# Performance work log

Hardware: AMD Instinct MI355X
Metric: run time of the kernel (lower is better)

The kernel has to match this reference:

```python
import jax, jax.numpy as jnp
import numpy as np

N_NODES = 100_000
N_EDGES = 1_600_000
DIM_IN = 256
ADD_TO_EDGE_SCORE = 0.5  # PyG EdgePooling default


def setup_inputs() -> dict:
    key = jax.random.key(0)
    k1, k2, k3 = jax.random.split(key, 3)
    x = jax.random.normal(k1, (N_NODES, DIM_IN), dtype=jnp.float32)
    edge_index = jax.random.randint(k2, (2, N_EDGES), 0, N_NODES, dtype=jnp.int32)
    batch = jnp.zeros((N_NODES,), dtype=jnp.int32)  # single graph
    W = jax.random.normal(k3, (2 * DIM_IN, 1), dtype=jnp.float32) / np.sqrt(2.0 * DIM_IN)
    b = jnp.zeros((1,), dtype=jnp.float32)
    return {"x": x, "edge_index": edge_index, "batch": batch, "W": W, "b": b}


def _segment_softmax(scores, seg, num_segments):
    m = jax.ops.segment_max(scores, seg, num_segments=num_segments)
    ex = jnp.exp(scores - m[seg])
    s = jax.ops.segment_sum(ex, seg, num_segments=num_segments)
    return ex / s[seg]


def _greedy_matching(rank, src, dst, num_nodes):
    """Maximal matching equivalent to sequential greedy over edges sorted by
    ascending rank (rank = position in descending-score argsort, a strict total
    order). Implemented as parallel locally-dominant matching rounds."""
    big = jnp.iinfo(jnp.int32).max

    def cond(state):
        alive, matched, chosen = state
        return jnp.any(alive)

    def body(state):
        alive, matched, chosen = state
        r = jnp.where(alive, rank, big)
        node_min = jnp.full((num_nodes,), big, dtype=jnp.int32)
        node_min = node_min.at[src].min(r)
        node_min = node_min.at[dst].min(r)
        # an alive edge is picked if it dominates all alive edges at both endpoints
        pick = alive & (rank == node_min[src]) & (rank == node_min[dst])
        matched = matched.at[jnp.where(pick, src, num_nodes)].set(True, mode='drop')
        matched = matched.at[jnp.where(pick, dst, num_nodes)].set(True, mode='drop')
        chosen = chosen | pick
        alive = alive & ~matched[src] & ~matched[dst]
        return alive, matched, chosen

    alive0 = jnp.ones_like(rank, dtype=bool)
    matched0 = jnp.zeros((num_nodes,), dtype=bool)
    chosen0 = jnp.zeros_like(alive0)
    _, matched, chosen = jax.lax.while_loop(cond, body, (alive0, matched0, chosen0))
    return chosen, matched


def reference(x, edge_index, batch, W, b):
    num_nodes, feat = x.shape
    num_edges = edge_index.shape[1]
    src, dst = edge_index[0], edge_index[1]

    # Linear([x_src || x_dst]) split to avoid materializing [E, 2F]
    s_src = x @ W[:feat, 0]   # [N]
    s_dst = x @ W[feat:, 0]   # [N]
    raw = s_src[src] + s_dst[dst] + b[0]            # [E]
    # dropout is identity in eval mode
    e = _segment_softmax(raw, dst, num_nodes) + ADD_TO_EDGE_SCORE  # [E]

    # rank: position of each edge in descending-score order
    order = jnp.argsort(-e)
    rank = jnp.zeros((num_edges,), dtype=jnp.int32).at[order].set(
        jnp.arange(num_edges, dtype=jnp.int32))

    chosen, matched = _greedy_matching(rank, src, dst, num_nodes)

    # cluster id of each chosen edge = its position among chosen edges in score order
    chosen_sorted = chosen[order]
    cid_sorted = jnp.cumsum(chosen_sorted.astype(jnp.int32)) - 1
    cid = jnp.zeros((num_edges,), dtype=jnp.int32).at[order].set(cid_sorted)
    num_matched = jnp.sum(chosen.astype(jnp.int32))

    # node -> cluster assignment; unmatched nodes get trailing singleton clusters
    cluster = jnp.zeros((num_nodes,), dtype=jnp.int32)
    cluster = cluster.at[jnp.where(chosen, src, num_nodes)].set(cid, mode='drop')
    cluster = cluster.at[jnp.where(chosen, dst, num_nodes)].set(cid, mode='drop')
    unm = num_matched + jnp.cumsum((~matched).astype(jnp.int32)) - 1
    cluster = jnp.where(matched, cluster, unm)
    num_clusters = num_matched + jnp.sum((~matched).astype(jnp.int32))

    # per-cluster score: chosen-edge scores for merged pairs, 1.0 for singletons
    new_edge_score = jnp.ones((num_nodes,), dtype=x.dtype)
    new_edge_score = new_edge_score.at[jnp.where(chosen, cid, num_nodes)].set(e, mode='drop')

    # scatter-merge node features (rows >= num_clusters are zero padding)
    new_x = jax.ops.segment_sum(x, cluster, num_segments=num_nodes)
    new_x = new_x * new_edge_score[:, None]

    new_edge_index = cluster[edge_index]  # remapped edges (coalesce/dedup omitted)
    new_batch = jnp.zeros((num_nodes,), dtype=batch.dtype).at[cluster].set(batch)

    return new_x, new_edge_index, new_batch, num_clusters
```

## Files before the change

### kernel.cpp

```cpp
#include <hip/hip_runtime.h>

typedef unsigned int u32;
typedef unsigned long long u64;
typedef unsigned char u8;

static constexpr int SORTN = 65536;
static constexpr int STILE = 2048;
static constexpr int NR    = 20;
static constexpr int NHEAVY= 3;
static constexpr int NXCD  = 8;

__device__ __forceinline__ u32 xccid() {
  u32 x;
  asm volatile("s_getreg_b32 %0, hwreg(HW_REG_XCC_ID)" : "=s"(x));
  return x & (NXCD - 1);
}

__device__ __forceinline__ void wmin64(u64* p, u64 v) {
  __hip_atomic_fetch_min(p, v, __ATOMIC_RELAXED, __HIP_MEMORY_SCOPE_WORKGROUP);
}
__device__ __forceinline__ void waddf64(double* p, double v) {
  __hip_atomic_fetch_add(p, v, __ATOMIC_RELAXED, __HIP_MEMORY_SCOPE_WORKGROUP);
}

typedef __attribute__((ext_vector_type(4))) float evf4;
template <typename T>
__device__ __forceinline__ T ntl(const T* p) { return __builtin_nontemporal_load(p); }
template <typename T>
__device__ __forceinline__ void nts(T v, T* p) { __builtin_nontemporal_store(v, p); }
__device__ __forceinline__ float4 ntl4(const float4* p) {
  evf4 v = __builtin_nontemporal_load((const evf4*)p);
  return make_float4(v.x, v.y, v.z, v.w);
}
__device__ __forceinline__ void nts4(float4 v, float4* p) {
  evf4 t; t.x = v.x; t.y = v.y; t.z = v.z; t.w = v.w;
  __builtin_nontemporal_store(t, (evf4*)p);
}

__device__ __forceinline__ u32 ordf(float f) {
  u32 u = __float_as_uint(f);
  return (u & 0x80000000u) ? ~u : (u | 0x80000000u);
}
__device__ __forceinline__ float inv_ordf(u32 m) {
  return __uint_as_float((m & 0x80000000u) ? (m ^ 0x80000000u) : ~m);
}

__global__ __launch_bounds__(256)
void k_init(double* ssum, double* ss8, u8* matched,
            u64* node_min, u64* nm8, float* scoreC, ulonglong2* sortbuf,
            u32* fcnt, u32* scalars, int N, int E) {
  int i = blockIdx.x * blockDim.x + threadIdx.x;
  if (i < N) { ssum[i] = 0.0; matched[i] = 0; scoreC[i] = 1.0f; }
  if (i < 2 * N) node_min[i] = ~0ull;
  if (i < NXCD * N) { nm8[i] = ~0ull; ss8[i] = 0.0; }
  if (i < SORTN) sortbuf[i] = make_ulonglong2(~0ull, ~0ull);
  if (i < 256)   fcnt[i] = 0u;
  if (i < 16)    scalars[i] = 0u;
  if (i == 0)    fcnt[0] = (u32)E;
}

__global__ __launch_bounds__(256)
void k_dots(const float4* __restrict__ x4, const float4* __restrict__ W4,
            float* __restrict__ s_src, float* __restrict__ s_dst, int N) {
  int gt = blockIdx.x * blockDim.x + threadIdx.x;
  int w = gt >> 6, lane = gt & 63;
  if (w >= N) return;
  float4 xa = ntl4(&x4[(size_t)w * 64 + lane]);
  float4 wa = W4[lane];
  float4 wb = W4[64 + lane];
  float pa = xa.x*wa.x + xa.y*wa.y + xa.z*wa.z + xa.w*wa.w;
  float pb = xa.x*wb.x + xa.y*wb.y + xa.z*wb.z + xa.w*wb.w;
  #pragma unroll
  for (int m = 32; m >= 1; m >>= 1) {
    pa += __shfl_xor(pa, m);
    pb += __shfl_xor(pb, m);
  }
  if (lane == 0) { s_src[w] = pa; s_dst[w] = pb; }
}

__global__ __launch_bounds__(256)
void k_esum(const int* __restrict__ src, const int* __restrict__ dst,
            const float* __restrict__ s_src, const float* __restrict__ s_dst,
            const float* __restrict__ bvec, double* ss8,
            float* __restrict__ exv, u64* __restrict__ frontS, int N, int E) {
  int e = blockIdx.x * blockDim.x + threadIdx.x;
  if (e >= E) return;
  double* sW = ss8 + (size_t)xccid() * N;
  int s = ntl(&src[e]), d = ntl(&dst[e]);
  float r = s_src[s] + s_dst[d] + bvec[0];
  float ex = expf(r);
  nts(ex, &exv[e]);
  nts(((u64)(u32)s << 32) | (u32)d, &frontS[e]);
  waddf64(&sW[d], (double)ex);
}

__global__ __launch_bounds__(256)
void k_ssmerge(const double* __restrict__ ss8, double* __restrict__ ssum, int N) {
  int v = blockIdx.x * 256 + threadIdx.x;
  if (v >= N) return;
  double s = 0.0;
  #pragma unroll
  for (int x = 0; x < NXCD; x++) s += ss8[(size_t)x * N + v];
  ssum[v] = s;
}

__global__ __launch_bounds__(256)
void k_scorekey(const u64* __restrict__ frontS, const float* __restrict__ exv,
                const double* __restrict__ ssum,
                u64* __restrict__ frontK, u64* nm8, int N, int E) {
  int e = blockIdx.x * blockDim.x + threadIdx.x;
  if (e >= E) return;
  u64* nmW = nm8 + (size_t)xccid() * N;
  u64 sd = ntl(&frontS[e]);
  int s = (int)(sd >> 32), d = (int)(u32)sd;
  float es = ntl(&exv[e]) / (float)ssum[d] + 0.5f;
  u64 key = ((u64)(~ordf(es)) << 32) | (u32)e;
  nts(key, &frontK[e]);
  wmin64(&nmW[s], key);
  if (d != s) wmin64(&nmW[d], key);
}

__global__ __launch_bounds__(256)
void k_merge(u64* nm8, u64* __restrict__ nmOut, int N) {
  int v = blockIdx.x * 256 + threadIdx.x;
  if (v >= N) return;
  u64 m = ~0ull;
  #pragma unroll
  for (int x = 0; x < NXCD; x++) {
    size_t idx = (size_t)x * N + v;
    u64 t = nm8[idx];
    if (t != ~0ull) { nm8[idx] = ~0ull; m = (t < m) ? t : m; }
  }
  nmOut[v] = m;
}

template<int R>
__global__ __launch_bounds__(256)
void k_mmin_h(const u64* __restrict__ fK, const u64* __restrict__ fS,
              const u32* __restrict__ cntp, const u8* __restrict__ matched,
              u64* nm8, int N) {
  u32 cnt = *cntp;
  u64* nmW = nm8 + (size_t)xccid() * N;
  u32 nth = gridDim.x * 256;
  for (u32 i = blockIdx.x * 256 + threadIdx.x; i < cnt; i += nth) {
    u64 sd = ntl(&fS[i]);
    int s = (int)(sd >> 32), d = (int)(u32)sd;
    if (matched[s] | matched[d]) continue;
    u64 k = ntl(&fK[i]);
    wmin64(&nmW[s], k);
    if (d != s) wmin64(&nmW[d], k);
  }
}

template<int R>
__global__ __launch_bounds__(256)
void k_mmin_l(const u64* __restrict__ fK, const u64* __restrict__ fS,
              const u32* __restrict__ cntp, const u8* __restrict__ matched,
              u64* nm) {
  u32 cnt = *cntp;
  u32 nth = gridDim.x * 256;
  for (u32 i = blockIdx.x * 256 + threadIdx.x; i < cnt; i += nth) {
    u64 sd = ntl(&fS[i]);
    int s = (int)(sd >> 32), d = (int)(u32)sd;
    if (matched[s] | matched[d]) continue;
    u64 k = ntl(&fK[i]);
    atomicMin(&nm[s], k);
    if (d != s) atomicMin(&nm[d], k);
  }
}

template<int R>
__global__ __launch_bounds__(256)
void k_mpick(const u64* __restrict__ fKin, const u64* __restrict__ fSin,
             const u32* __restrict__ cntp, const u64* __restrict__ nm,
             u64* nmNext, u8* matched, u64* fKout, u64* fSout, u32* cntOut,
             ulonglong2* sortbuf, u32* scalars) {
  __shared__ u32 wb[4];
  __shared__ u32 bbase;
  u32 cnt = *cntp;
  int tx = threadIdx.x, lane = tx & 63, wid = tx >> 6;
  for (u32 base = blockIdx.x * 256; base < cnt; base += gridDim.x * 256) {
    u32 gid = base + tx;
    u64 k = 0, sd = 0;
    int s = 0, d = 0;
    bool pk = false, surv = false;
    if (gid < cnt) {
      k = ntl(&fKin[gid]); sd = ntl(&fSin[gid]);
      s = (int)(sd >> 32); d = (int)(u32)sd;
      if (!(matched[s] | matched[d])) {
        pk = (nm[s] == k) && (nm[d] == k);
        surv = !pk;
      }
    }
    u64 pm = __ballot(pk);
    if (pm) {
      u32 pre = (u32)__popcll(pm & ((1ull << lane) - 1ull));
      int ldr = __ffsll((long long)pm) - 1;
      u32 pb = 0;
      if (lane == ldr) pb = atomicAdd(&scalars[0], (u32)__popcll(pm));
      pb = __shfl(pb, ldr);
      if (pk) { matched[s] = 1; matched[d] = 1; sortbuf[pb + pre] = make_ulonglong2(k, sd); }
    }
    u64 sm = __ballot(surv);
    if (lane == 0) wb[wid] = (u32)__popcll(sm);
    __syncthreads();
    if (tx == 0) {
      u32 tt = wb[0] + wb[1] + wb[2] + wb[3];
      bbase = tt ? atomicAdd(cntOut, tt) : 0u;
    }
    __syncthreads();
    if (surv) {
      u32 woff = 0;
      for (int w = 0; w < wid; w++) woff += wb[w];
      u32 pre = (u32)__popcll(sm & ((1ull << lane) - 1ull));
      u32 o = bbase + woff + pre;
      nts(k, &fKout[o]);
      nts(sd, &fSout[o]);
      nmNext[s] = ~0ull;
      if (d != s) nmNext[d] = ~0ull;
    }
    __syncthreads();
  }
}

__global__ __launch_bounds__(1024)
void k_mfinish(u64* fKA, u64* fSA, u64* fKB, u64* fSB, u8* matched,
               u64* nmA, u64* nmB, ulonglong2* sortbuf,
               const u32* __restrict__ cntp, u32* scalars) {
  __shared__ u32 sh_cnt;
  u32 cnt = *cntp;
  int tx = threadIdx.x;
  u64 *fKin = fKA, *fSin = fSA, *fKout = fKB, *fSout = fSB;
  u64 *nmCur = nmA, *nmNxt = nmB;
  while (cnt > 0) {
    if (tx == 0) sh_cnt = 0;
    __syncthreads();
    for (u32 i = tx; i < cnt; i += 1024) {
      u64 sd = fSin[i];
      int s = (int)(sd >> 32), d = (int)(u32)sd;
      if (matched[s] | matched[d]) continue;
      u64 k = fKin[i];
      wmin64(&nmCur[s], k);
      if (d != s) wmin64(&nmCur[d], k);
    }
    __syncthreads();
    for (u32 i = tx; i < cnt; i += 1024) {
      u64 sd = fSin[i];
      int s = (int)(sd >> 32), d = (int)(u32)sd;
      if (matched[s] | matched[d]) continue;
      u64 k = fKin[i];
      u64 a = __hip_atomic_fetch_add(&nmCur[s], 0ull, __ATOMIC_RELAXED,
                                     __HIP_MEMORY_SCOPE_WORKGROUP);
      u64 b = (d == s) ? a
            : __hip_atomic_fetch_add(&nmCur[d], 0ull, __ATOMIC_RELAXED,
                                     __HIP_MEMORY_SCOPE_WORKGROUP);
      if (a == k && b == k) {
        matched[s] = 1; matched[d] = 1;
        u32 o = atomicAdd(&scalars[0], 1u);
        sortbuf[o] = make_ulonglong2(k, sd);
      } else {
        u32 o = atomicAdd(&sh_cnt, 1u);
        fKout[o] = k; fSout[o] = sd;
        nmNxt[s] = ~0ull;
        if (d != s) nmNxt[d] = ~0ull;
      }
    }
    __syncthreads();
    cnt = sh_cnt;
    u64* t;
    t = fKin; fKin = fKout; fKout = t;
    t = fSin; fSin = fSout; fSout = t;
    t = nmCur; nmCur = nmNxt; nmNxt = t;
    __syncthreads();
  }
}

__global__ __launch_bounds__(1024)
void k_sort1(ulonglong2* buf) {
  __shared__ ulonglong2 t[STILE];
  const int base = blockIdx.x * STILE;
  for (int i = threadIdx.x; i < STILE; i += 1024) t[i] = buf[base + i];
  __syncthreads();
  for (int k = 2; k <= STILE; k <<= 1) {
    for (int j = k >> 1; j > 0; j >>= 1) {
      for (int i = threadIdx.x; i < STILE; i += 1024) {
        int p = i ^ j;
        if (p > i) {
          bool dir = (((base + i) & k) == 0);
          ulonglong2 a = t[i], c = t[p];
          if ((a.x > c.x) == dir) { t[i] = c; t[p] = a; }
        }
      }
      __syncthreads();
    }
  }
  for (int i = threadIdx.x; i < STILE; i += 1024) buf[base + i] = t[i];
}

__global__ __launch_bounds__(256)
void k_gpass(ulonglong2* buf, int j, int k) {
  int i = blockIdx.x * 256 + threadIdx.x;
  int p = i ^ j;
  if (p > i && p < SORTN) {
    bool dir = ((i & k) == 0);
    ulonglong2 a = buf[i], c = buf[p];
    if ((a.x > c.x) == dir) { buf[i] = c; buf[p] = a; }
  }
}

__global__ __launch_bounds__(1024)
void k_sortl(ulonglong2* buf, int k) {
  __shared__ ulonglong2 t[STILE];
  const int base = blockIdx.x * STILE;
  const bool dir = ((base & k) == 0);
  for (int i = threadIdx.x; i < STILE; i += 1024) t[i] = buf[base + i];
  __syncthreads();
  for (int j = STILE >> 1; j > 0; j >>= 1) {
    for (int i = threadIdx.x; i < STILE; i += 1024) {
      int p = i ^ j;
      if (p > i) {
        ulonglong2 a = t[i], c = t[p];
        if ((a.x > c.x) == dir) { t[i] = c; t[p] = a; }
      }
    }
    __syncthreads();
  }
  for (int i = threadIdx.x; i < STILE; i += 1024) buf[base + i] = t[i];
}

__global__ __launch_bounds__(256)
void k_assign(const ulonglong2* __restrict__ buf,
              int* cluster, int* memA, int* memB, float* scoreC,
              const u32* __restrict__ scalars) {
  int i = blockIdx.x * blockDim.x + threadIdx.x;
  if (i >= (int)scalars[0]) return;
  ulonglong2 t = buf[i];
  int s = (int)(t.y >> 32), d = (int)(u32)t.y;
  cluster[s] = i; cluster[d] = i;
  scoreC[i] = inv_ordf(~(u32)(t.x >> 32));
  memA[i] = s;
  memB[i] = (s == d) ? -1 : d;
}

__global__ __launch_bounds__(256)
void k_scan1(const u8* __restrict__ matched, u32* partials, int N) {
  __shared__ u32 sh[256];
  int b = blockIdx.x, tx = threadIdx.x;
  int v0 = b * 1024 + tx * 4;
  u32 c = 0;
  #pragma unroll
  for (int q = 0; q < 4; q++) { int v = v0 + q; if (v < N && !matched[v]) c++; }
  sh[tx] = c; __syncthreads();
  for (int s = 128; s > 0; s >>= 1) { if (tx < s) sh[tx] += sh[tx + s]; __syncthreads(); }
  if (tx == 0) partials[b] = sh[0];
}

__global__ void k_scan2(const u32* partials, u32* partials2, u32* scalars, int NB) {
  if (blockIdx.x == 0 && threadIdx.x == 0) {
    u32 run = 0;
    for (int i = 0; i < NB; i++) { partials2[i] = run; run += partials[i]; }
    scalars[1] = run;
    scalars[2] = scalars[0] + run;
  }
}

__global__ __launch_bounds__(256)
void k_scan3(const u8* __restrict__ matched, const u32* __restrict__ partials2,
             const u32* __restrict__ scalars, int* cluster, int* memA, int* memB, int N) {
  __shared__ u32 sh[256];
  int b = blockIdx.x, tx = threadIdx.x;
  int v0 = b * 1024 + tx * 4;
  u32 f[4]; u32 c = 0;
  #pragma unroll
  for (int q = 0; q < 4; q++) { int v = v0 + q; f[q] = (v < N && !matched[v]); c += f[q]; }
  sh[tx] = c; __syncthreads();
  for (int s = 1; s < 256; s <<= 1) {
    u32 x = sh[tx];
    u32 y = (tx >= s) ? sh[tx - s] : 0;
    __syncthreads();
    sh[tx] = x + y;
    __syncthreads();
  }
  u32 base = scalars[0] + partials2[b] + (sh[tx] - c);
  #pragma unroll
  for (int q = 0; q < 4; q++) {
    if (f[q]) {
      int v = v0 + q;
      int cc = (int)base++;
      cluster[v] = cc; memA[cc] = v; memB[cc] = -1;
    }
  }
}

__global__ __launch_bounds__(256)
void k_newx(const float4* __restrict__ x4, const int* __restrict__ memA,
            const int* __restrict__ memB, const float* __restrict__ scoreC,
            const u32* __restrict__ scalars, float4* __restrict__ out4, int N) {
  int gt = blockIdx.x * blockDim.x + threadIdx.x;
  int w = gt >> 6, lane = gt & 63;
  if (w >= N) return;
  int nc = (int)scalars[2];
  float4 o;
  if (w < nc) {
    int a = memA[w], b = memB[w];
    float s = scoreC[w];
    float4 va = ntl4(&x4[(size_t)a * 64 + lane]);
    float ox = va.x, oy = va.y, oz = va.z, ow = va.w;
    if (b >= 0) {
      float4 vb = ntl4(&x4[(size_t)b * 64 + lane]);
      ox += vb.x; oy += vb.y; oz += vb.z; ow += vb.w;
    }
    o = make_float4(ox * s, oy * s, oz * s, ow * s);
  } else {
    o = make_float4(0.f, 0.f, 0.f, 0.f);
  }
  nts4(o, &out4[(size_t)w * 64 + lane]);
}

__global__ __launch_bounds__(256)
void k_remap(const int* __restrict__ ei, const int* __restrict__ cluster,
             float* __restrict__ outE, float* __restrict__ outB,
             const u32* __restrict__ scalars, int twoE, int N) {
  int i = blockIdx.x * blockDim.x + threadIdx.x;
  if (i < twoE) nts((float)cluster[ntl(&ei[i])], &outE[i]);
  int j = i - twoE;
  if (j >= 0 && j < N) outB[j] = 0.0f;
  if (j == N) outB[N] = (float)scalars[2];
}

template<int R>
static void launch_rounds(u64* fKA, u64* fSA, u64* fKB, u64* fSB, u64* nm8,
                          u64* node_min, u8* matched, ulonglong2* sortbuf,
                          u32* fcnt, u32* scalars, int N, int NB_E,
                          hipStream_t stream) {
  if constexpr (R < NR) {
    u64* fKin  = (R & 1) ? fKB : fKA;
    u64* fSin  = (R & 1) ? fSB : fSA;
    u64* fKout = (R & 1) ? fKA : fKB;
    u64* fSout = (R & 1) ? fSA : fSB;
    u64* nm  = node_min + (size_t)(R & 1) * N;
    u64* nmN = node_min + (size_t)((R & 1) ^ 1) * N;
    int nbr = (R < 30) ? (NB_E >> R) : 0; if (nbr < 64) nbr = 64;
    if constexpr (R == 0) {
    } else if constexpr (R < NHEAVY) {
      k_mmin_h<R><<<nbr, 256, 0, stream>>>(fKin, fSin, fcnt + R, matched, nm8, N);
      k_merge<<<(N + 255) / 256, 256, 0, stream>>>(nm8, nm, N);
    } else {
      k_mmin_l<R><<<nbr, 256, 0, stream>>>(fKin, fSin, fcnt + R, matched, nm);
    }
    k_mpick<R><<<nbr, 256, 0, stream>>>(fKin, fSin, fcnt + R, nm, nmN, matched,
                                        fKout, fSout, fcnt + R + 1, sortbuf, scalars);
    launch_rounds<R + 1>(fKA, fSA, fKB, fSB, nm8, node_min, matched, sortbuf,
                         fcnt, scalars, N, NB_E, stream);
  }
}

extern "C" void kernel_launch(void* const* d_in, const int* in_sizes, int n_in,
                              void* d_out, int out_size, void* d_ws, size_t ws_size,
                              hipStream_t stream) {
  const float* x    = (const float*)d_in[0];
  const int*   ei   = (const int*)d_in[1];
  const float* W    = (const float*)d_in[3];
  const float* bvec = (const float*)d_in[4];
  int N = in_sizes[2];
  int E = in_sizes[1] / 2;

  char* p = (char*)d_ws;
  auto alloc = [&](size_t bytes) { char* r = p; p += (bytes + 255) & ~(size_t)255; return r; };
  float*      s_src    = (float*)alloc((size_t)N * 4);
  float*      s_dst    = (float*)alloc((size_t)N * 4);
  double*     ssum     = (double*)alloc((size_t)N * 8);
  double*     ss8      = (double*)alloc((size_t)NXCD * N * 8);
  float*      exv      = (float*)alloc((size_t)E * 4);
  u64*        fKA      = (u64*)alloc((size_t)E * 8);
  u64*        fSA      = (u64*)alloc((size_t)E * 8);
  u64*        fKB      = (u64*)alloc((size_t)E * 8);
  u64*        fSB      = (u64*)alloc((size_t)E * 8);
  u8*         matched  = (u8*)alloc((size_t)N);
  u64*        node_min = (u64*)alloc((size_t)2 * N * 8);
  u64*        nm8      = (u64*)alloc((size_t)NXCD * N * 8);
  ulonglong2* sortbuf  = (ulonglong2*)alloc((size_t)SORTN * 16);
  int*        cluster  = (int*)alloc((size_t)N * 4);
  int*        memA     = (int*)alloc((size_t)N * 4);
  int*        memB     = (int*)alloc((size_t)N * 4);
  float*      scoreC   = (float*)alloc((size_t)N * 4);
  u32*        fcnt     = (u32*)alloc(1024);
  u32*        partials = (u32*)alloc(4096);
  u32*        partials2= (u32*)alloc(4096);
  u32*        scalars  = (u32*)alloc(256);
  (void)ws_size; (void)out_size; (void)n_in;

  const int* srcp = ei;
  const int* dstp = ei + E;
  float* out  = (float*)d_out;
  float* outX = out;
  float* outE = out + (size_t)N * 256;
  float* outB = outE + (size_t)2 * E;

  int NB_E = (E + 255) / 256;
  int cover = NXCD * N; if (cover < SORTN) cover = SORTN;
  k_init<<<(cover + 255) / 256, 256, 0, stream>>>(ssum, ss8, matched,
                                                  node_min, nm8, scoreC, sortbuf,
                                                  fcnt, scalars, N, E);
  k_dots<<<((size_t)N * 64 + 255) / 256, 256, 0, stream>>>(
      (const float4*)x, (const float4*)W, s_src, s_dst, N);
  k_esum<<<NB_E, 256, 0, stream>>>(srcp, dstp, s_src, s_dst, bvec, ss8,
                                   exv, fSA, N, E);
  k_ssmerge<<<(N + 255) / 256, 256, 0, stream>>>(ss8, ssum, N);
  k_scorekey<<<NB_E, 256, 0, stream>>>(fSA, exv, ssum, fKA, nm8, N, E);
  k_merge<<<(N + 255) / 256, 256, 0, stream>>>(nm8, node_min, N);

  launch_rounds<0>(fKA, fSA, fKB, fSB, nm8, node_min, matched, sortbuf,
                   fcnt, scalars, N, NB_E, stream);
  k_mfinish<<<1, 1024, 0, stream>>>(fKA, fSA, fKB, fSB, matched,
                                    node_min, node_min + N,
                                    sortbuf, fcnt + NR, scalars);

  k_sort1<<<SORTN / STILE, 1024, 0, stream>>>(sortbuf);
  for (int k = STILE << 1; k <= SORTN; k <<= 1) {
    for (int j = k >> 1; j >= STILE; j >>= 1)
      k_gpass<<<SORTN / 256, 256, 0, stream>>>(sortbuf, j, k);
    k_sortl<<<SORTN / STILE, 1024, 0, stream>>>(sortbuf, k);
  }

  k_assign<<<SORTN / 256, 256, 0, stream>>>(sortbuf, cluster, memA, memB, scoreC, scalars);
  int NB = (N + 1023) / 1024;
  k_scan1<<<NB, 256, 0, stream>>>(matched, partials, N);
  k_scan2<<<1, 64, 0, stream>>>(partials, partials2, scalars, NB);
  k_scan3<<<NB, 256, 0, stream>>>(matched, partials2, scalars, cluster, memA, memB, N);

  k_newx<<<((size_t)N * 64 + 255) / 256, 256, 0, stream>>>(
      (const float4*)x, memA, memB, scoreC, scalars, (float4*)outX, N);
  k_remap<<<(2 * E + N + 1 + 255) / 256, 256, 0, stream>>>(
      ei, cluster, outE, outB, scalars, 2 * E, N);
}
```

Baseline: 1.357 ms.

## Recompute edge keys on the fly and pack src/dst/id into one frontier word

Stops materializing the per-edge exp values and the separate key and src/dst frontier arrays. Edge scores are recomputed from the per-node dot products and softmax sums wherever a key is needed, and the frontier becomes one 64-bit word packing src (bits 38+), dst (17 bits) and edge id (21 bits). Round 0 reads edge_index directly, and the scan2 kernel is folded into scan3 so each block sums the partials itself. This removes several E-sized streams of writes and reads in exchange for repeated gathers, exp and divide per round. The packing assumes node ids fit in 17 bits and edge ids in 21 bits, which holds for the given sizes only.

```diff
diff --git a/kernel.cpp b/kernel.cpp
--- a/kernel.cpp
+++ b/kernel.cpp
@@ -9,6 +9,10 @@
 static constexpr int NR    = 20;
 static constexpr int NHEAVY= 3;
 static constexpr int NXCD  = 8;
+
+__device__ __forceinline__ u64 packsde(int s, int d, u32 e) {
+  return ((u64)(u32)s << 38) | ((u64)(u32)d << 21) | e;
+}
 
 __device__ __forceinline__ u32 xccid() {
   u32 x;
@@ -43,6 +47,13 @@
 }
 __device__ __forceinline__ float inv_ordf(u32 m) {
   return __uint_as_float((m & 0x80000000u) ? (m ^ 0x80000000u) : ~m);
+}
+
+__device__ __forceinline__ u64 edge_key(int s, int d, u32 e,
+    const float* __restrict__ s_src, const float* __restrict__ s_dst,
+    float b, const double* __restrict__ ssum) {
+  float es = expf(s_src[s] + s_dst[d] + b) / (float)ssum[d] + 0.5f;
+  return ((u64)(~ordf(es)) << 32) | e;
 }
 
 __global__ __launch_bounds__(256)
@@ -56,7 +67,6 @@
   if (i < SORTN) sortbuf[i] = make_ulonglong2(~0ull, ~0ull);
   if (i < 256)   fcnt[i] = 0u;
   if (i < 16)    scalars[i] = 0u;
-  if (i == 0)    fcnt[0] = (u32)E;
 }
 
 __global__ __launch_bounds__(256)
@@ -81,16 +91,12 @@
 __global__ __launch_bounds__(256)
 void k_esum(const int* __restrict__ src, const int* __restrict__ dst,
             const float* __restrict__ s_src, const float* __restrict__ s_dst,
-            const float* __restrict__ bvec, double* ss8,
-            float* __restrict__ exv, u64* __restrict__ frontS, int N, int E) {
+            const float* __restrict__ bvec, double* ss8, int N, int E) {
   int e = blockIdx.x * blockDim.x + threadIdx.x;
   if (e >= E) return;
   double* sW = ss8 + (size_t)xccid() * N;
   int s = ntl(&src[e]), d = ntl(&dst[e]);
-  float r = s_src[s] + s_dst[d] + bvec[0];
-  float ex = expf(r);
-  nts(ex, &exv[e]);
-  nts(((u64)(u32)s << 32) | (u32)d, &frontS[e]);
+  float ex = expf(s_src[s] + s_dst[d] + bvec[0]);
   waddf64(&sW[d], (double)ex);
 }
 
@@ -105,17 +111,15 @@
 }
 
 __global__ __launch_bounds__(256)
-void k_scorekey(const u64* __restrict__ frontS, const float* __restrict__ exv,
-                const double* __restrict__ ssum,
-                u64* __restrict__ frontK, u64* nm8, int N, int E) {
+void k_keymin(const int* __restrict__ src, const int* __restrict__ dst,
+              const float* __restrict__ s_src, const float* __restrict__ s_dst,
+              const float* __restrict__ bvec, const double* __restrict__ ssum,
+              u64* nm8, int N, int E) {
   int e = blockIdx.x * blockDim.x + threadIdx.x;
   if (e >= E) return;
   u64* nmW = nm8 + (size_t)xccid() * N;
-  u64 sd = ntl(&frontS[e]);
-  int s = (int)(sd >> 32), d = (int)(u32)sd;
-  float es = ntl(&exv[e]) / (float)ssum[d] + 0.5f;
-  u64 key = ((u64)(~ordf(es)) << 32) | (u32)e;
-  nts(key, &frontK[e]);
+  int s = ntl(&src[e]), d = ntl(&dst[e]);
+  u64 key = edge_key(s, d, (u32)e, s_src, s_dst, bvec[0], ssum);
   wmin64(&nmW[s], key);
   if (d != s) wmin64(&nmW[d], key);
 }
@@ -136,17 +140,20 @@
 
 template<int R>
 __global__ __launch_bounds__(256)
-void k_mmin_h(const u64* __restrict__ fK, const u64* __restrict__ fS,
-              const u32* __restrict__ cntp, const u8* __restrict__ matched,
+void k_mmin_h(const u64* __restrict__ fin, const u32* __restrict__ cntp,
+              const u8* __restrict__ matched,
+              const float* __restrict__ s_src, const float* __restrict__ s_dst,
+              const float* __restrict__ bvec, const double* __restrict__ ssum,
               u64* nm8, int N) {
   u32 cnt = *cntp;
   u64* nmW = nm8 + (size_t)xccid() * N;
   u32 nth = gridDim.x * 256;
+  float b = bvec[0];
   for (u32 i = blockIdx.x * 256 + threadIdx.x; i < cnt; i += nth) {
-    u64 sd = ntl(&fS[i]);
-    int s = (int)(sd >> 32), d = (int)(u32)sd;
+    u64 p = ntl(&fin[i]);
+    int s = (int)(p >> 38), d = (int)((p >> 21) & 0x1FFFF);
     if (matched[s] | matched[d]) continue;
-    u64 k = ntl(&fK[i]);
+    u64 k = edge_key(s, d, (u32)(p & 0x1FFFFF), s_src, s_dst, b, ssum);
     wmin64(&nmW[s], k);
     if (d != s) wmin64(&nmW[d], k);
   }
@@ -154,16 +161,19 @@
 
 template<int R>
 __global__ __launch_bounds__(256)
-void k_mmin_l(const u64* __restrict__ fK, const u64* __restrict__ fS,
-              const u32* __restrict__ cntp, const u8* __restrict__ matched,
+void k_mmin_l(const u64* __restrict__ fin, const u32* __restrict__ cntp,
+              const u8* __restrict__ matched,
+              const float* __restrict__ s_src, const float* __restrict__ s_dst,
+              const float* __restrict__ bvec, const double* __restrict__ ssum,
               u64* nm) {
   u32 cnt = *cntp;
   u32 nth = gridDim.x * 256;
+  float b = bvec[0];
   for (u32 i = blockIdx.x * 256 + threadIdx.x; i < cnt; i += nth) {
-    u64 sd = ntl(&fS[i]);
-    int s = (int)(sd >> 32), d = (int)(u32)sd;
+    u64 p = ntl(&fin[i]);
+    int s = (int)(p >> 38), d = (int)((p >> 21) & 0x1FFFF);
     if (matched[s] | matched[d]) continue;
-    u64 k = ntl(&fK[i]);
+    u64 k = edge_key(s, d, (u32)(p & 0x1FFFFF), s_src, s_dst, b, ssum);
     atomicMin(&nm[s], k);
     if (d != s) atomicMin(&nm[d], k);
   }
@@ -171,23 +181,32 @@
 
 template<int R>
 __global__ __launch_bounds__(256)
-void k_mpick(const u64* __restrict__ fKin, const u64* __restrict__ fSin,
-             const u32* __restrict__ cntp, const u64* __restrict__ nm,
-             u64* nmNext, u8* matched, u64* fKout, u64* fSout, u32* cntOut,
-             ulonglong2* sortbuf, u32* scalars) {
+void k_mpick(const int* __restrict__ src, const int* __restrict__ dst,
+             const u64* __restrict__ fin, const u32* __restrict__ cntp,
+             const float* __restrict__ s_src, const float* __restrict__ s_dst,
+             const float* __restrict__ bvec, const double* __restrict__ ssum,
+             const u64* __restrict__ nm, u64* nmNext, u8* matched,
+             u64* fout, u32* cntOut, ulonglong2* sortbuf, u32* scalars, int E) {
   __shared__ u32 wb[4];
   __shared__ u32 bbase;
-  u32 cnt = *cntp;
+  u32 cnt = (R == 0) ? (u32)E : *cntp;
+  float b = bvec[0];
   int tx = threadIdx.x, lane = tx & 63, wid = tx >> 6;
   for (u32 base = blockIdx.x * 256; base < cnt; base += gridDim.x * 256) {
     u32 gid = base + tx;
-    u64 k = 0, sd = 0;
+    u64 k = 0, p = 0;
     int s = 0, d = 0;
     bool pk = false, surv = false;
     if (gid < cnt) {
-      k = ntl(&fKin[gid]); sd = ntl(&fSin[gid]);
-      s = (int)(sd >> 32); d = (int)(u32)sd;
+      if (R == 0) {
+        s = ntl(&src[gid]); d = ntl(&dst[gid]);
+        p = packsde(s, d, gid);
+      } else {
+        p = ntl(&fin[gid]);
+        s = (int)(p >> 38); d = (int)((p >> 21) & 0x1FFFF);
+      }
       if (!(matched[s] | matched[d])) {
+        k = edge_key(s, d, (u32)(p & 0x1FFFFF), s_src, s_dst, b, ssum);
         pk = (nm[s] == k) && (nm[d] == k);
         surv = !pk;
       }
@@ -199,7 +218,7 @@
       u32 pb = 0;
       if (lane == ldr) pb = atomicAdd(&scalars[0], (u32)__popcll(pm));
       pb = __shfl(pb, ldr);
-      if (pk) { matched[s] = 1; matched[d] = 1; sortbuf[pb + pre] = make_ulonglong2(k, sd); }
+      if (pk) { matched[s] = 1; matched[d] = 1; sortbuf[pb + pre] = make_ulonglong2(k, p); }
     }
     u64 sm = __ballot(surv);
     if (lane == 0) wb[wid] = (u32)__popcll(sm);
@@ -213,9 +232,7 @@
       u32 woff = 0;
       for (int w = 0; w < wid; w++) woff += wb[w];
       u32 pre = (u32)__popcll(sm & ((1ull << lane) - 1ull));
-      u32 o = bbase + woff + pre;
-      nts(k, &fKout[o]);
-      nts(sd, &fSout[o]);
+      nts(p, &fout[bbase + woff + pre]);
       nmNext[s] = ~0ull;
       if (d != s) nmNext[d] = ~0ull;
     }
@@ -224,43 +241,45 @@
 }
 
 __global__ __launch_bounds__(1024)
-void k_mfinish(u64* fKA, u64* fSA, u64* fKB, u64* fSB, u8* matched,
-               u64* nmA, u64* nmB, ulonglong2* sortbuf,
-               const u32* __restrict__ cntp, u32* scalars) {
+void k_mfinish(u64* fA, u64* fB, u8* matched, u64* nmA, u64* nmB,
+               const float* __restrict__ s_src, const float* __restrict__ s_dst,
+               const float* __restrict__ bvec, const double* __restrict__ ssum,
+               ulonglong2* sortbuf, const u32* __restrict__ cntp, u32* scalars) {
   __shared__ u32 sh_cnt;
   u32 cnt = *cntp;
   int tx = threadIdx.x;
-  u64 *fKin = fKA, *fSin = fSA, *fKout = fKB, *fSout = fSB;
+  float b = bvec[0];
+  u64 *fin = fA, *fout = fB;
   u64 *nmCur = nmA, *nmNxt = nmB;
   while (cnt > 0) {
     if (tx == 0) sh_cnt = 0;
     __syncthreads();
     for (u32 i = tx; i < cnt; i += 1024) {
-      u64 sd = fSin[i];
-      int s = (int)(sd >> 32), d = (int)(u32)sd;
+      u64 p = fin[i];
+      int s = (int)(p >> 38), d = (int)((p >> 21) & 0x1FFFF);
       if (matched[s] | matched[d]) continue;
-      u64 k = fKin[i];
+      u64 k = edge_key(s, d, (u32)(p & 0x1FFFFF), s_src, s_dst, b, ssum);
       wmin64(&nmCur[s], k);
       if (d != s) wmin64(&nmCur[d], k);
     }
     __syncthreads();
     for (u32 i = tx; i < cnt; i += 1024) {
-      u64 sd = fSin[i];
-      int s = (int)(sd >> 32), d = (int)(u32)sd;
+      u64 p = fin[i];
+      int s = (int)(p >> 38), d = (int)((p >> 21) & 0x1FFFF);
       if (matched[s] | matched[d]) continue;
-      u64 k = fKin[i];
+      u64 k = edge_key(s, d, (u32)(p & 0x1FFFFF), s_src, s_dst, b, ssum);
       u64 a = __hip_atomic_fetch_add(&nmCur[s], 0ull, __ATOMIC_RELAXED,
                                      __HIP_MEMORY_SCOPE_WORKGROUP);
-      u64 b = (d == s) ? a
-            : __hip_atomic_fetch_add(&nmCur[d], 0ull, __ATOMIC_RELAXED,
-                                     __HIP_MEMORY_SCOPE_WORKGROUP);
-      if (a == k && b == k) {
+      u64 bb = (d == s) ? a
+             : __hip_atomic_fetch_add(&nmCur[d], 0ull, __ATOMIC_RELAXED,
+                                      __HIP_MEMORY_SCOPE_WORKGROUP);
+      if (a == k && bb == k) {
         matched[s] = 1; matched[d] = 1;
         u32 o = atomicAdd(&scalars[0], 1u);
-        sortbuf[o] = make_ulonglong2(k, sd);
+        sortbuf[o] = make_ulonglong2(k, p);
       } else {
         u32 o = atomicAdd(&sh_cnt, 1u);
-        fKout[o] = k; fSout[o] = sd;
+        fout[o] = p;
         nmNxt[s] = ~0ull;
         if (d != s) nmNxt[d] = ~0ull;
       }
@@ -268,8 +287,7 @@
     __syncthreads();
     cnt = sh_cnt;
     u64* t;
-    t = fKin; fKin = fKout; fKout = t;
-    t = fSin; fSin = fSout; fSout = t;
+    t = fin; fin = fout; fout = t;
     t = nmCur; nmCur = nmNxt; nmNxt = t;
     __syncthreads();
   }
@@ -335,7 +353,7 @@
   int i = blockIdx.x * blockDim.x + threadIdx.x;
   if (i >= (int)scalars[0]) return;
   ulonglong2 t = buf[i];
-  int s = (int)(t.y >> 32), d = (int)(u32)t.y;
+  int s = (int)(t.y >> 38), d = (int)((t.y >> 21) & 0x1FFFF);
   cluster[s] = i; cluster[d] = i;
   scoreC[i] = inv_ordf(~(u32)(t.x >> 32));
   memA[i] = s;
@@ -355,20 +373,17 @@
   if (tx == 0) partials[b] = sh[0];
 }
 
-__global__ void k_scan2(const u32* partials, u32* partials2, u32* scalars, int NB) {
-  if (blockIdx.x == 0 && threadIdx.x == 0) {
-    u32 run = 0;
-    for (int i = 0; i < NB; i++) { partials2[i] = run; run += partials[i]; }
-    scalars[1] = run;
-    scalars[2] = scalars[0] + run;
-  }
-}
-
-__global__ __launch_bounds__(256)
-void k_scan3(const u8* __restrict__ matched, const u32* __restrict__ partials2,
-             const u32* __restrict__ scalars, int* cluster, int* memA, int* memB, int N) {
+__global__ __launch_bounds__(256)
+void k_scan3(const u8* __restrict__ matched, const u32* __restrict__ partials,
+             u32* scalars, int* cluster, int* memA, int* memB, int N, int NB) {
   __shared__ u32 sh[256];
   int b = blockIdx.x, tx = threadIdx.x;
+  u32 pre = 0, total = 0;
+  for (int i = 0; i < NB; i++) { u32 v = partials[i]; if (i < b) pre += v; total += v; }
+  if (b == 0 && tx == 0) {
+    scalars[1] = total;
+    scalars[2] = scalars[0] + total;
+  }
   int v0 = b * 1024 + tx * 4;
   u32 f[4]; u32 c = 0;
   #pragma unroll
@@ -381,7 +396,7 @@
     sh[tx] = x + y;
     __syncthreads();
   }
-  u32 base = scalars[0] + partials2[b] + (sh[tx] - c);
+  u32 base = scalars[0] + pre + (sh[tx] - c);
   #pragma unroll
   for (int q = 0; q < 4; q++) {
     if (f[q]) {
@@ -429,29 +444,35 @@
 }
 
 template<int R>
-static void launch_rounds(u64* fKA, u64* fSA, u64* fKB, u64* fSB, u64* nm8,
-                          u64* node_min, u8* matched, ulonglong2* sortbuf,
-                          u32* fcnt, u32* scalars, int N, int NB_E,
+static void launch_rounds(const int* srcp, const int* dstp,
+                          u64* fA, u64* fB, u64* nm8, u64* node_min,
+                          u8* matched, ulonglong2* sortbuf,
+                          const float* s_src, const float* s_dst,
+                          const float* bvec, const double* ssum,
+                          u32* fcnt, u32* scalars, int N, int E, int NB_E,
                           hipStream_t stream) {
   if constexpr (R < NR) {
-    u64* fKin  = (R & 1) ? fKB : fKA;
-    u64* fSin  = (R & 1) ? fSB : fSA;
-    u64* fKout = (R & 1) ? fKA : fKB;
-    u64* fSout = (R & 1) ? fSA : fSB;
+    u64* fin  = (R & 1) ? fB : fA;
+    u64* fout = (R & 1) ? fA : fB;
     u64* nm  = node_min + (size_t)(R & 1) * N;
     u64* nmN = node_min + (size_t)((R & 1) ^ 1) * N;
     int nbr = (R < 30) ? (NB_E >> R) : 0; if (nbr < 64) nbr = 64;
     if constexpr (R == 0) {
     } else if constexpr (R < NHEAVY) {
-      k_mmin_h<R><<<nbr, 256, 0, stream>>>(fKin, fSin, fcnt + R, matched, nm8, N);
+      k_mmin_h<R><<<nbr, 256, 0, stream>>>(fin, fcnt + R, matched,
+                                           s_src, s_dst, bvec, ssum, nm8, N);
       k_merge<<<(N + 255) / 256, 256, 0, stream>>>(nm8, nm, N);
     } else {
-      k_mmin_l<R><<<nbr, 256, 0, stream>>>(fKin, fSin, fcnt + R, matched, nm);
-    }
-    k_mpick<R><<<nbr, 256, 0, stream>>>(fKin, fSin, fcnt + R, nm, nmN, matched,
-                                        fKout, fSout, fcnt + R + 1, sortbuf, scalars);
-    launch_rounds<R + 1>(fKA, fSA, fKB, fSB, nm8, node_min, matched, sortbuf,
-                         fcnt, scalars, N, NB_E, stream);
+      k_mmin_l<R><<<nbr, 256, 0, stream>>>(fin, fcnt + R, matched,
+                                           s_src, s_dst, bvec, ssum, nm);
+    }
+    k_mpick<R><<<nbr, 256, 0, stream>>>(srcp, dstp, fin, fcnt + R,
+                                        s_src, s_dst, bvec, ssum,
+                                        nm, nmN, matched, fout, fcnt + R + 1,
+                                        sortbuf, scalars, E);
+    launch_rounds<R + 1>(srcp, dstp, fA, fB, nm8, node_min, matched, sortbuf,
+                         s_src, s_dst, bvec, ssum, fcnt, scalars, N, E, NB_E,
+                         stream);
   }
 }
 
@@ -471,11 +492,8 @@
   float*      s_dst    = (float*)alloc((size_t)N * 4);
   double*     ssum     = (double*)alloc((size_t)N * 8);
   double*     ss8      = (double*)alloc((size_t)NXCD * N * 8);
-  float*      exv      = (float*)alloc((size_t)E * 4);
-  u64*        fKA      = (u64*)alloc((size_t)E * 8);
-  u64*        fSA      = (u64*)alloc((size_t)E * 8);
-  u64*        fKB      = (u64*)alloc((size_t)E * 8);
-  u64*        fSB      = (u64*)alloc((size_t)E * 8);
+  u64*        fA       = (u64*)alloc((size_t)E * 8);
+  u64*        fB       = (u64*)alloc((size_t)E * 8);
   u8*         matched  = (u8*)alloc((size_t)N);
   u64*        node_min = (u64*)alloc((size_t)2 * N * 8);
   u64*        nm8      = (u64*)alloc((size_t)NXCD * N * 8);
@@ -486,7 +504,6 @@
   float*      scoreC   = (float*)alloc((size_t)N * 4);
   u32*        fcnt     = (u32*)alloc(1024);
   u32*        partials = (u32*)alloc(4096);
-  u32*        partials2= (u32*)alloc(4096);
   u32*        scalars  = (u32*)alloc(256);
   (void)ws_size; (void)out_size; (void)n_in;
 
@@ -504,16 +521,16 @@
                                                   fcnt, scalars, N, E);
   k_dots<<<((size_t)N * 64 + 255) / 256, 256, 0, stream>>>(
       (const float4*)x, (const float4*)W, s_src, s_dst, N);
-  k_esum<<<NB_E, 256, 0, stream>>>(srcp, dstp, s_src, s_dst, bvec, ss8,
-                                   exv, fSA, N, E);
+  k_esum<<<NB_E, 256, 0, stream>>>(srcp, dstp, s_src, s_dst, bvec, ss8, N, E);
   k_ssmerge<<<(N + 255) / 256, 256, 0, stream>>>(ss8, ssum, N);
-  k_scorekey<<<NB_E, 256, 0, stream>>>(fSA, exv, ssum, fKA, nm8, N, E);
+  k_keymin<<<NB_E, 256, 0, stream>>>(srcp, dstp, s_src, s_dst, bvec, ssum,
+                                     nm8, N, E);
   k_merge<<<(N + 255) / 256, 256, 0, stream>>>(nm8, node_min, N);
 
-  launch_rounds<0>(fKA, fSA, fKB, fSB, nm8, node_min, matched, sortbuf,
-                   fcnt, scalars, N, NB_E, stream);
-  k_mfinish<<<1, 1024, 0, stream>>>(fKA, fSA, fKB, fSB, matched,
-                                    node_min, node_min + N,
+  launch_rounds<0>(srcp, dstp, fA, fB, nm8, node_min, matched, sortbuf,
+                   s_src, s_dst, bvec, ssum, fcnt, scalars, N, E, NB_E, stream);
+  k_mfinish<<<1, 1024, 0, stream>>>(fA, fB, matched, node_min, node_min + N,
+                                    s_src, s_dst, bvec, ssum,
                                     sortbuf, fcnt + NR, scalars);
 
   k_sort1<<<SORTN / STILE, 1024, 0, stream>>>(sortbuf);
@@ -526,8 +543,7 @@
   k_assign<<<SORTN / 256, 256, 0, stream>>>(sortbuf, cluster, memA, memB, scoreC, scalars);
   int NB = (N + 1023) / 1024;
   k_scan1<<<NB, 256, 0, stream>>>(matched, partials, N);
-  k_scan2<<<1, 64, 0, stream>>>(partials, partials2, scalars, NB);
-  k_scan3<<<NB, 256, 0, stream>>>(matched, partials2, scalars, cluster, memA, memB, N);
+  k_scan3<<<NB, 256, 0, stream>>>(matched, partials, scalars, cluster, memA, memB, N, NB);
 
   k_newx<<<((size_t)N * 64 + 255) / 256, 256, 0, stream>>>(
       (const float4*)x, memA, memB, scoreC, scalars, (float4*)outX, N);
```

Result: no change. 1.343 ms (-1.0%).
